# Optimization experiments

Hardware: AMD Instinct MI355X
Metric: run time of the kernel (lower is better)

Reference implementation:

```python
import jax, jax.numpy as jnp
import numpy as np

N_NODES = 100000


def _add_self_loops(edge_index, edge_weight, num_nodes):
    # PyG gcn_norm default: add self-loops with weight 1.0
    loop = jnp.arange(num_nodes, dtype=edge_index.dtype)
    row = jnp.concatenate([edge_index[0], loop])
    col = jnp.concatenate([edge_index[1], loop])
    ew = jnp.concatenate([edge_weight, jnp.ones((num_nodes,), edge_weight.dtype)])
    return row, col, ew


def _gcn_norm(row, col, ew, num_nodes):
    # deg[j] = sum of incoming edge weights (col = target, source_to_target flow)
    deg = jax.ops.segment_sum(ew, col, num_segments=num_nodes)
    dinv = jnp.where(deg > 0, jax.lax.rsqrt(deg), 0.0)
    return dinv[row] * ew * dinv[col]


def _gcn_conv(x, W, b, row, col, norm, num_nodes):
    h = x @ W                                  # [N, F_out] small dense GEMM
    msg = norm[:, None] * h[row]               # gather + scale  [E, F_out]
    out = jax.ops.segment_sum(msg, col, num_segments=num_nodes)  # scatter-add
    return out + b


def setup_inputs() -> dict:
    key = jax.random.key(0)
    ks = jax.random.split(key, 6)
    N, E, F_in, H, C = N_NODES, 3200000, 512, 16, 10
    x = jax.random.normal(ks[0], (N, F_in), dtype=jnp.float32)
    edge_index = jax.random.randint(ks[1], (2, E), 0, N, dtype=jnp.int64)
    edge_weight = jax.random.uniform(ks[2], (E,), dtype=jnp.float32)
    W1 = jax.random.normal(ks[3], (F_in, H), dtype=jnp.float32) * (1.0 / np.sqrt(F_in))
    b1 = jnp.zeros((H,), jnp.float32)
    W2 = jax.random.normal(ks[4], (H, C), dtype=jnp.float32) * (1.0 / np.sqrt(H))
    b2 = jnp.zeros((C,), jnp.float32)
    return {"x": x, "edge_index": edge_index, "edge_weight": edge_weight,
            "W1": W1, "b1": b1, "W2": W2, "b2": b2}


def reference(x, edge_index, edge_weight, W1, b1, W2, b2):
    N = x.shape[0]
    row, col, ew = _add_self_loops(edge_index, edge_weight, N)
    norm = _gcn_norm(row, col, ew, N)          # cached=True: same norm both layers
    x1 = _gcn_conv(x, W1, b1, row, col, norm, N)
    h = jax.nn.relu(x1)                        # dropout is identity in eval mode
    logits = _gcn_conv(h, W2, b2, row, col, norm, N)
    return jax.nn.log_softmax(logits, axis=1), x1
```

## Files before the change

kernel.cpp:

```cpp
#include <hip/hip_runtime.h>
#include <hip/hip_bf16.h>


#define NF1 16
#define NF2 10
#define FIN 512
#define EPB 8192
#define SK  4

typedef unsigned long long ull;
typedef unsigned short us;

__device__ __forceinline__ us f2bf(float f) {
    union { float f; unsigned u; } v; v.f = f;
    unsigned r = v.u + 0x7FFFu + ((v.u >> 16) & 1u);
    return (us)(r >> 16);
}
__device__ __forceinline__ float bf2f(us h) {
    union { unsigned u; float f; } v; v.u = ((unsigned)h) << 16;
    return v.f;
}
__device__ __forceinline__ float w15f(unsigned e) {
    union { unsigned u; float f; } v; v.u = (e >> 17) << 16;
    return v.f;
}

__global__ __launch_bounds__(256) void coarse_count_kernel(const int* __restrict__ col,
                                                           int* __restrict__ blkhist,
                                                           int E, int NB, int NBLK) {
    __shared__ int lh[256];
    int t = threadIdx.x;
    lh[t] = 0;
    __syncthreads();
    int base = blockIdx.x * EPB;
    int cnt = min(EPB, E - base);
    for (int i = t; i < cnt; i += 256)
        atomicAdd(&lh[col[base + i] >> 9], 1);
    __syncthreads();
    if (t < NB) blkhist[t * NBLK + blockIdx.x] = lh[t];
}

__global__ __launch_bounds__(512) void bucket_scan_kernel(int* __restrict__ blkhist,
                                                          int* __restrict__ btot,
                                                          int NBLK) {
    __shared__ int s[512];
    int t = threadIdx.x;
    int* p = blkhist + (size_t)blockIdx.x * NBLK;
    int carry = 0;
    for (int base = 0; base < NBLK; base += 512) {
        int idx = base + t;
        int v = (idx < NBLK) ? p[idx] : 0;
        s[t] = v;
        __syncthreads();
        for (int off = 1; off < 512; off <<= 1) {
            int u = (t >= off) ? s[t - off] : 0;
            __syncthreads();
            s[t] += u;
            __syncthreads();
        }
        if (idx < NBLK) p[idx] = s[t] - v + carry;
        carry += s[511];
        __syncthreads();
    }
    if (t == 0) btot[blockIdx.x] = carry;
}

__global__ __launch_bounds__(256) void base_scan_kernel(const int* __restrict__ btot,
                                                        int* __restrict__ bbase,
                                                        int* __restrict__ rowptr,
                                                        int NB, int E, int N) {
    __shared__ int s[256];
    int t = threadIdx.x;
    int v = (t < NB) ? btot[t] : 0;
    s[t] = v;
    __syncthreads();
    for (int off = 1; off < 256; off <<= 1) {
        int u = (t >= off) ? s[t - off] : 0;
        __syncthreads();
        s[t] += u;
        __syncthreads();
    }
    if (t < NB) bbase[t] = s[t] - v;
    if (t == 0) { bbase[NB] = E; rowptr[N] = E; }
}

__global__ __launch_bounds__(256) void coarse_scatter_kernel(const int* __restrict__ row,
                                                             const int* __restrict__ col,
                                                             const float* __restrict__ ew,
                                                             const int* __restrict__ blkhist,
                                                             const int* __restrict__ bbase,
                                                             ull* __restrict__ pool,
                                                             int E, int NB, int NBLK) {
    __shared__ int cur[256];
    int t = threadIdx.x;
    if (t < NB) cur[t] = blkhist[t * NBLK + blockIdx.x] + bbase[t];
    __syncthreads();
    int base = blockIdx.x * EPB;
    int cnt = min(EPB, E - base);
    for (int i = t; i < cnt; i += 256) {
        int e = base + i;
        int c = col[e], r = row[e];
        float w = ew[e];
        int b = c >> 9, c9 = c & 511;
        int pos = atomicAdd(&cur[b], 1);
        pool[pos] = ((ull)((((unsigned)c9) << 20) | (unsigned)r) << 32) | (ull)__float_as_uint(w);
    }
}

__global__ __launch_bounds__(1024) void fine_sort_kernel(const ull* __restrict__ pool,
                                                         const int* __restrict__ bbase,
                                                         unsigned* __restrict__ csr,
                                                         int* __restrict__ rowptr,
                                                         float* __restrict__ dinv, int N) {
    __shared__ int hist[512];
    __shared__ float wsum[512];
    __shared__ int cur[512];
    int t = threadIdx.x;
    int b = blockIdx.x;
    int bb = bbase[b], be = bbase[b + 1];
    int Ki = be - bb;
    if (t < 512) { hist[t] = 0; wsum[t] = 0.0f; }
    __syncthreads();
    int i = t;
    for (; i + 3 * 1024 < Ki; i += 4 * 1024) {
        ull p0 = pool[bb + i];
        ull p1 = pool[bb + i + 1024];
        ull p2 = pool[bb + i + 2048];
        ull p3 = pool[bb + i + 3072];
        unsigned h0 = (unsigned)(p0 >> 32), h1 = (unsigned)(p1 >> 32);
        unsigned h2 = (unsigned)(p2 >> 32), h3 = (unsigned)(p3 >> 32);
        atomicAdd(&hist[(h0 >> 20) & 511], 1);
        atomicAdd(&wsum[(h0 >> 20) & 511], __uint_as_float((unsigned)p0));
        atomicAdd(&hist[(h1 >> 20) & 511], 1);
        atomicAdd(&wsum[(h1 >> 20) & 511], __uint_as_float((unsigned)p1));
        atomicAdd(&hist[(h2 >> 20) & 511], 1);
        atomicAdd(&wsum[(h2 >> 20) & 511], __uint_as_float((unsigned)p2));
        atomicAdd(&hist[(h3 >> 20) & 511], 1);
        atomicAdd(&wsum[(h3 >> 20) & 511], __uint_as_float((unsigned)p3));
    }
    for (; i < Ki; i += 1024) {
        ull p = pool[bb + i];
        unsigned hi = (unsigned)(p >> 32);
        int c9 = (hi >> 20) & 511;
        atomicAdd(&hist[c9], 1);
        atomicAdd(&wsum[c9], __uint_as_float((unsigned)p));
    }
    __syncthreads();
    int own = (t < 512) ? hist[t] : 0;
    if (t < 512) cur[t] = own;
    __syncthreads();
    for (int off = 1; off < 512; off <<= 1) {
        int v = (t >= off && t < 512) ? cur[t - off] : 0;
        __syncthreads();
        if (t < 512) cur[t] += v;
        __syncthreads();
    }
    int excl = (t < 512) ? (cur[t] - own) : 0;
    if (t < 512) cur[t] = excl;
    int c = (b << 9) + t;
    if (t < 512 && c < N) {
        rowptr[c] = bb + excl;
        dinv[c] = rsqrtf(1.0f + wsum[t]);
    }
    __syncthreads();
    i = t;
    for (; i + 3 * 1024 < Ki; i += 4 * 1024) {
        ull p0 = pool[bb + i];
        ull p1 = pool[bb + i + 1024];
        ull p2 = pool[bb + i + 2048];
        ull p3 = pool[bb + i + 3072];
#pragma unroll
        for (int j = 0; j < 4; j++) {
            ull p = (j == 0) ? p0 : (j == 1) ? p1 : (j == 2) ? p2 : p3;
            unsigned hi = (unsigned)(p >> 32);
            int c9 = (hi >> 20) & 511;
            unsigned r = hi & 0xFFFFFu;
            unsigned lo = (unsigned)p;
            unsigned w15 = (lo + 0x8000u) >> 16;
            int k = atomicAdd(&cur[c9], 1);
            csr[bb + k] = (w15 << 17) | r;
        }
    }
    for (; i < Ki; i += 1024) {
        ull p = pool[bb + i];
        unsigned hi = (unsigned)(p >> 32);
        int c9 = (hi >> 20) & 511;
        unsigned r = hi & 0xFFFFFu;
        unsigned lo = (unsigned)p;
        unsigned w15 = (lo + 0x8000u) >> 16;
        int k = atomicAdd(&cur[c9], 1);
        csr[bb + k] = (w15 << 17) | r;
    }
}

__device__ __forceinline__ void fma16(float av, const float* __restrict__ wrow,
                                      float* __restrict__ acc) {
#pragma unroll
    for (int f = 0; f < NF1; f++) acc[f] = fmaf(av, wrow[f], acc[f]);
}

__global__ __launch_bounds__(256) void gemm1_kernel(const float* __restrict__ x,
                                                    const float* __restrict__ W1,
                                                    float* __restrict__ part,
                                                    int N, int nbRow) {
    int b = blockIdx.x;
    int q = b / nbRow;
    int rb = b - q * nbRow;
    int row = rb * 256 + threadIdx.x;
    if (row >= N) return;
    const int k0 = q * (FIN / SK);

    float acc[NF1];
#pragma unroll
    for (int f = 0; f < NF1; f++) acc[f] = 0.0f;

    const float* xr = x + (size_t)row * FIN + k0;
    const float* wp = W1 + (size_t)k0 * NF1;

#pragma unroll 2
    for (int k = 0; k < FIN / SK; k += 16) {
        const float4* xp = reinterpret_cast<const float4*>(xr + k);
        float4 a0 = xp[0];
        float4 a1 = xp[1];
        float4 a2 = xp[2];
        float4 a3 = xp[3];
        const float* wk = wp + (size_t)k * NF1;
        fma16(a0.x, wk + 0 * NF1, acc);
        fma16(a0.y, wk + 1 * NF1, acc);
        fma16(a0.z, wk + 2 * NF1, acc);
        fma16(a0.w, wk + 3 * NF1, acc);
        fma16(a1.x, wk + 4 * NF1, acc);
        fma16(a1.y, wk + 5 * NF1, acc);
        fma16(a1.z, wk + 6 * NF1, acc);
        fma16(a1.w, wk + 7 * NF1, acc);
        fma16(a2.x, wk + 8 * NF1, acc);
        fma16(a2.y, wk + 9 * NF1, acc);
        fma16(a2.z, wk + 10 * NF1, acc);
        fma16(a2.w, wk + 11 * NF1, acc);
        fma16(a3.x, wk + 12 * NF1, acc);
        fma16(a3.y, wk + 13 * NF1, acc);
        fma16(a3.z, wk + 14 * NF1, acc);
        fma16(a3.w, wk + 15 * NF1, acc);
    }

    float* pp = part + ((size_t)q * N + row) * NF1;
#pragma unroll
    for (int qq = 0; qq < 4; qq++) {
        float4 o = make_float4(acc[4 * qq], acc[4 * qq + 1], acc[4 * qq + 2], acc[4 * qq + 3]);
        *reinterpret_cast<float4*>(pp + 4 * qq) = o;
    }
}

__global__ __launch_bounds__(256) void combine_scale_kernel(const float* __restrict__ part,
                                                            const float* __restrict__ dinv,
                                                            us* __restrict__ hs16, int N) {
    int i4 = blockIdx.x * 256 + threadIdx.x;
    int total = N * NF1 / 4;
    if (i4 >= total) return;
    int rowIdx = i4 >> 2;
    const float4* p0 = reinterpret_cast<const float4*>(part);
    const float4* p1 = reinterpret_cast<const float4*>(part + (size_t)1 * N * NF1);
    const float4* p2 = reinterpret_cast<const float4*>(part + (size_t)2 * N * NF1);
    const float4* p3 = reinterpret_cast<const float4*>(part + (size_t)3 * N * NF1);
    float4 a = p0[i4], b = p1[i4], c = p2[i4], d4 = p3[i4];
    float d = dinv[rowIdx];
    ushort4 u;
    u.x = f2bf(d * (a.x + b.x + c.x + d4.x));
    u.y = f2bf(d * (a.y + b.y + c.y + d4.y));
    u.z = f2bf(d * (a.z + b.z + c.z + d4.z));
    u.w = f2bf(d * (a.w + b.w + c.w + d4.w));
    reinterpret_cast<ushort4*>(hs16)[i4] = u;
}

__global__ __launch_bounds__(256) void gather1_kernel(const unsigned* __restrict__ csr,
                                                      const int* __restrict__ rowptr,
                                                      const float* __restrict__ dinv,
                                                      const us* __restrict__ hs16,
                                                      const float* __restrict__ b1,
                                                      float* __restrict__ x1, int N) {
    int t = blockIdx.x * 256 + threadIdx.x;
    int node = t >> 4, f = t & 15;
    if (node >= N) return;
    int s = rowptr[node], e = rowptr[node + 1];
    float di = dinv[node];
    float acc = bf2f(hs16[(size_t)node * NF1 + f]);
    int i = s;
    for (; i + 7 < e; i += 8) {
        unsigned e0 = csr[i],     e1 = csr[i + 1], e2 = csr[i + 2], e3 = csr[i + 3];
        unsigned e4 = csr[i + 4], e5 = csr[i + 5], e6 = csr[i + 6], e7 = csr[i + 7];
        float h0 = bf2f(hs16[(size_t)(e0 & 0x1FFFF) * NF1 + f]);
        float h1 = bf2f(hs16[(size_t)(e1 & 0x1FFFF) * NF1 + f]);
        float h2 = bf2f(hs16[(size_t)(e2 & 0x1FFFF) * NF1 + f]);
        float h3 = bf2f(hs16[(size_t)(e3 & 0x1FFFF) * NF1 + f]);
        float h4 = bf2f(hs16[(size_t)(e4 & 0x1FFFF) * NF1 + f]);
        float h5 = bf2f(hs16[(size_t)(e5 & 0x1FFFF) * NF1 + f]);
        float h6 = bf2f(hs16[(size_t)(e6 & 0x1FFFF) * NF1 + f]);
        float h7 = bf2f(hs16[(size_t)(e7 & 0x1FFFF) * NF1 + f]);
        acc += w15f(e0) * h0;
        acc += w15f(e1) * h1;
        acc += w15f(e2) * h2;
        acc += w15f(e3) * h3;
        acc += w15f(e4) * h4;
        acc += w15f(e5) * h5;
        acc += w15f(e6) * h6;
        acc += w15f(e7) * h7;
    }
    for (; i < e; i++) {
        unsigned e0 = csr[i];
        acc += w15f(e0) * bf2f(hs16[(size_t)(e0 & 0x1FFFF) * NF1 + f]);
    }
    x1[(size_t)node * NF1 + f] = b1[f] + di * acc;
}

__global__ __launch_bounds__(256) void gemm2_kernel(const float* __restrict__ x1,
                                                    const float* __restrict__ W2,
                                                    const float* __restrict__ dinv,
                                                    us* __restrict__ hh16, int N) {
    int j = blockIdx.x * 256 + threadIdx.x;
    if (j >= N) return;
    float xr[NF1];
#pragma unroll
    for (int f = 0; f < NF1; f++) xr[f] = fmaxf(x1[(size_t)j * NF1 + f], 0.0f);
    float d = dinv[j];
    float o[NF2];
#pragma unroll
    for (int c = 0; c < NF2; c++) {
        float acc = 0.0f;
#pragma unroll
        for (int f = 0; f < NF1; f++) acc += xr[f] * W2[f * NF2 + c];
        o[c] = d * acc;
    }
    unsigned* hp = reinterpret_cast<unsigned*>(const_cast<us*>(hh16) + (size_t)j * NF2);
#pragma unroll
    for (int cp = 0; cp < 5; cp++)
        hp[cp] = (unsigned)f2bf(o[2 * cp]) | ((unsigned)f2bf(o[2 * cp + 1]) << 16);
}

__global__ __launch_bounds__(256) void gather2_lsm_kernel(const unsigned* __restrict__ csr,
                                                          const int* __restrict__ rowptr,
                                                          const float* __restrict__ dinv,
                                                          const us* __restrict__ hh16,
                                                          const float* __restrict__ b2,
                                                          float* __restrict__ out, int N) {
    int t = blockIdx.x * 256 + threadIdx.x;
    int node = t >> 4, f = t & 15;
    bool act = (node < N) && (f < NF2);
    float acc = 0.0f;
    if (node < N) {
        int s = rowptr[node], e = rowptr[node + 1];
        float di = dinv[node];
        acc = act ? bf2f(hh16[(size_t)node * NF2 + f]) : 0.0f;
        int i = s;
        if (f < NF2) {
            for (; i + 7 < e; i += 8) {
                unsigned e0 = csr[i],     e1 = csr[i + 1], e2 = csr[i + 2], e3 = csr[i + 3];
                unsigned e4 = csr[i + 4], e5 = csr[i + 5], e6 = csr[i + 6], e7 = csr[i + 7];
                float h0 = bf2f(hh16[(size_t)(e0 & 0x1FFFF) * NF2 + f]);
                float h1 = bf2f(hh16[(size_t)(e1 & 0x1FFFF) * NF2 + f]);
                float h2 = bf2f(hh16[(size_t)(e2 & 0x1FFFF) * NF2 + f]);
                float h3 = bf2f(hh16[(size_t)(e3 & 0x1FFFF) * NF2 + f]);
                float h4 = bf2f(hh16[(size_t)(e4 & 0x1FFFF) * NF2 + f]);
                float h5 = bf2f(hh16[(size_t)(e5 & 0x1FFFF) * NF2 + f]);
                float h6 = bf2f(hh16[(size_t)(e6 & 0x1FFFF) * NF2 + f]);
                float h7 = bf2f(hh16[(size_t)(e7 & 0x1FFFF) * NF2 + f]);
                acc += w15f(e0) * h0;
                acc += w15f(e1) * h1;
                acc += w15f(e2) * h2;
                acc += w15f(e3) * h3;
                acc += w15f(e4) * h4;
                acc += w15f(e5) * h5;
                acc += w15f(e6) * h6;
                acc += w15f(e7) * h7;
            }
            for (; i < e; i++) {
                unsigned e0 = csr[i];
                acc += w15f(e0) * bf2f(hh16[(size_t)(e0 & 0x1FFFF) * NF2 + f]);
            }
        }
        acc = b2[f] + di * acc;
    }
    float m = act ? acc : -INFINITY;
#pragma unroll
    for (int off = 1; off < 16; off <<= 1) m = fmaxf(m, __shfl_xor(m, off, 16));
    float p = act ? expf(acc - m) : 0.0f;
    float ssum = p;
#pragma unroll
    for (int off = 1; off < 16; off <<= 1) ssum += __shfl_xor(ssum, off, 16);
    if (act) out[(size_t)node * NF2 + f] = acc - m - logf(ssum);
}

extern "C" void kernel_launch(void* const* d_in, const int* in_sizes, int n_in,
                              void* d_out, int out_size, void* d_ws, size_t ws_size,
                              hipStream_t stream) {
    const float* x  = (const float*)d_in[0];
    const int*   ei = (const int*)d_in[1];
    const float* ew = (const float*)d_in[2];
    const float* W1 = (const float*)d_in[3];
    const float* b1 = (const float*)d_in[4];
    const float* W2 = (const float*)d_in[5];
    const float* b2 = (const float*)d_in[6];

    const int E = in_sizes[2];
    const int N = in_sizes[0] / FIN;
    const int* row = ei;
    const int* col = ei + E;

    const int NB   = (N + 511) >> 9;
    const int NBLK = (E + EPB - 1) / EPB;

    float* out    = (float*)d_out;
    float* logits = out;
    float* x1     = out + (size_t)N * NF2;

    char* ws = (char*)d_ws;
    size_t off = 0;
    auto alloc = [&](size_t bytes) { void* p = ws + off; off += (bytes + 255) / 256 * 256; return p; };
    ull*      pool    = (ull*)     alloc((size_t)E * 8);
    unsigned* csr     = (unsigned*)alloc((size_t)E * 4);
    float*    part    = (float*)   alloc((size_t)SK * N * NF1 * 4);
    us*       hs16    = (us*)      alloc((size_t)N * NF1 * 2);
    us*       hh16    = (us*)      alloc((size_t)N * NF2 * 2 + 64);
    float*    dinv    = (float*)   alloc((size_t)N * 4);
    int*      rowptr  = (int*)     alloc((size_t)(N + 1) * 4);
    int*      blkhist = (int*)     alloc((size_t)NB * NBLK * 4);
    int*      btot    = (int*)     alloc((size_t)NB * 4);
    int*      bbase   = (int*)     alloc((size_t)(NB + 1) * 4);
    (void)ws_size; (void)n_in; (void)out_size;

    dim3 blk(256);
    int gN    = (N + 255) / 256;
    int g16   = (N + 15) / 16;
    int nbRow = (N + 255) / 256;

    coarse_count_kernel<<<NBLK, blk, 0, stream>>>(col, blkhist, E, NB, NBLK);
    bucket_scan_kernel<<<NB, dim3(512), 0, stream>>>(blkhist, btot, NBLK);
    base_scan_kernel<<<1, blk, 0, stream>>>(btot, bbase, rowptr, NB, E, N);
    coarse_scatter_kernel<<<NBLK, blk, 0, stream>>>(row, col, ew, blkhist, bbase, pool, E, NB, NBLK);
    fine_sort_kernel<<<NB, dim3(1024), 0, stream>>>(pool, bbase, csr, rowptr, dinv, N);

    gemm1_kernel<<<SK * nbRow, blk, 0, stream>>>(x, W1, part, N, nbRow);
    combine_scale_kernel<<<(N * NF1 / 4 + 255) / 256, blk, 0, stream>>>(part, dinv, hs16, N);
    gather1_kernel<<<g16, blk, 0, stream>>>(csr, rowptr, dinv, hs16, b1, x1, N);

    gemm2_kernel<<<gN, blk, 0, stream>>>(x1, W2, dinv, hh16, N);
    gather2_lsm_kernel<<<g16, blk, 0, stream>>>(csr, rowptr, dinv, hh16, b2, logits, N);
}
```

Before: 228.3 us.

## Fuse gemm2 into gather1 via shuffle reduction and halve GEMM1 K-split

The second-layer dense projection is folded into the first aggregation kernel. Each 16-lane group reduces relu(x1)·W2 with xor shuffles and writes the bf16 hidden row directly, which removes a kernel launch and the re-read of x1. Separately, the GEMM1 K-split drops from 4 to 2, so there are fewer partial buffers to write and combine, but each block does a longer reduction and there are half as many blocks. The fused path issues 10 shuffle reductions per node and adds those to the gather kernel.

```diff
diff --git a/kernel.cpp b/kernel.cpp
--- a/kernel.cpp
+++ b/kernel.cpp
@@ -6,7 +6,7 @@
 #define NF2 10
 #define FIN 512
 #define EPB 8192
-#define SK  4
+#define SK  2
 
 typedef unsigned long long ull;
 typedef unsigned short us;
@@ -204,7 +204,7 @@
                                                     float* __restrict__ part,
                                                     int N, int nbRow) {
     int b = blockIdx.x;
-    int q = b / nbRow;
+    int q = (b >= nbRow) ? 1 : 0;
     int rb = b - q * nbRow;
     int row = rb * 256 + threadIdx.x;
     if (row >= N) return;
@@ -259,25 +259,25 @@
     if (i4 >= total) return;
     int rowIdx = i4 >> 2;
     const float4* p0 = reinterpret_cast<const float4*>(part);
-    const float4* p1 = reinterpret_cast<const float4*>(part + (size_t)1 * N * NF1);
-    const float4* p2 = reinterpret_cast<const float4*>(part + (size_t)2 * N * NF1);
-    const float4* p3 = reinterpret_cast<const float4*>(part + (size_t)3 * N * NF1);
-    float4 a = p0[i4], b = p1[i4], c = p2[i4], d4 = p3[i4];
+    const float4* p1 = reinterpret_cast<const float4*>(part + (size_t)N * NF1);
+    float4 a = p0[i4], b = p1[i4];
     float d = dinv[rowIdx];
     ushort4 u;
-    u.x = f2bf(d * (a.x + b.x + c.x + d4.x));
-    u.y = f2bf(d * (a.y + b.y + c.y + d4.y));
-    u.z = f2bf(d * (a.z + b.z + c.z + d4.z));
-    u.w = f2bf(d * (a.w + b.w + c.w + d4.w));
+    u.x = f2bf(d * (a.x + b.x));
+    u.y = f2bf(d * (a.y + b.y));
+    u.z = f2bf(d * (a.z + b.z));
+    u.w = f2bf(d * (a.w + b.w));
     reinterpret_cast<ushort4*>(hs16)[i4] = u;
 }
 
-__global__ __launch_bounds__(256) void gather1_kernel(const unsigned* __restrict__ csr,
-                                                      const int* __restrict__ rowptr,
-                                                      const float* __restrict__ dinv,
-                                                      const us* __restrict__ hs16,
-                                                      const float* __restrict__ b1,
-                                                      float* __restrict__ x1, int N) {
+__global__ __launch_bounds__(256) void gather1_gemm2_kernel(const unsigned* __restrict__ csr,
+                                                            const int* __restrict__ rowptr,
+                                                            const float* __restrict__ dinv,
+                                                            const us* __restrict__ hs16,
+                                                            const float* __restrict__ b1,
+                                                            const float* __restrict__ W2,
+                                                            float* __restrict__ x1,
+                                                            us* __restrict__ hh16, int N) {
     int t = blockIdx.x * 256 + threadIdx.x;
     int node = t >> 4, f = t & 15;
     if (node >= N) return;
@@ -309,31 +309,19 @@
         unsigned e0 = csr[i];
         acc += w15f(e0) * bf2f(hs16[(size_t)(e0 & 0x1FFFF) * NF1 + f]);
     }
-    x1[(size_t)node * NF1 + f] = b1[f] + di * acc;
-}
-
-__global__ __launch_bounds__(256) void gemm2_kernel(const float* __restrict__ x1,
-                                                    const float* __restrict__ W2,
-                                                    const float* __restrict__ dinv,
-                                                    us* __restrict__ hh16, int N) {
-    int j = blockIdx.x * 256 + threadIdx.x;
-    if (j >= N) return;
-    float xr[NF1];
-#pragma unroll
-    for (int f = 0; f < NF1; f++) xr[f] = fmaxf(x1[(size_t)j * NF1 + f], 0.0f);
-    float d = dinv[j];
-    float o[NF2];
+    float x1v = b1[f] + di * acc;
+    x1[(size_t)node * NF1 + f] = x1v;
+
+    float xr = fmaxf(x1v, 0.0f);
+    float hhv = 0.0f;
 #pragma unroll
     for (int c = 0; c < NF2; c++) {
-        float acc = 0.0f;
-#pragma unroll
-        for (int f = 0; f < NF1; f++) acc += xr[f] * W2[f * NF2 + c];
-        o[c] = d * acc;
-    }
-    unsigned* hp = reinterpret_cast<unsigned*>(const_cast<us*>(hh16) + (size_t)j * NF2);
-#pragma unroll
-    for (int cp = 0; cp < 5; cp++)
-        hp[cp] = (unsigned)f2bf(o[2 * cp]) | ((unsigned)f2bf(o[2 * cp + 1]) << 16);
+        float v = xr * W2[f * NF2 + c];
+#pragma unroll
+        for (int off = 1; off < 16; off <<= 1) v += __shfl_xor(v, off, 16);
+        if (f == c) hhv = v;
+    }
+    if (f < NF2) hh16[(size_t)node * NF2 + f] = f2bf(di * hhv);
 }
 
 __global__ __launch_bounds__(256) void gather2_lsm_kernel(const unsigned* __restrict__ csr,
@@ -428,7 +416,6 @@
     (void)ws_size; (void)n_in; (void)out_size;
 
     dim3 blk(256);
-    int gN    = (N + 255) / 256;
     int g16   = (N + 15) / 16;
     int nbRow = (N + 255) / 256;
 
@@ -440,8 +427,7 @@
 
     gemm1_kernel<<<SK * nbRow, blk, 0, stream>>>(x, W1, part, N, nbRow);
     combine_scale_kernel<<<(N * NF1 / 4 + 255) / 256, blk, 0, stream>>>(part, dinv, hs16, N);
-    gather1_kernel<<<g16, blk, 0, stream>>>(csr, rowptr, dinv, hs16, b1, x1, N);
-
-    gemm2_kernel<<<gN, blk, 0, stream>>>(x1, W2, dinv, hh16, N);
+    gather1_gemm2_kernel<<<g16, blk, 0, stream>>>(csr, rowptr, dinv, hs16, b1, W2, x1, hh16, N);
+
     gather2_lsm_kernel<<<g16, blk, 0, stream>>>(csr, rowptr, dinv, hh16, b2, logits, N);
 }
```

Result: no change. 225.3 us (median of 2 runs) (-1.3%).
